# Optimization experiments

Hardware: AMD Instinct MI355X
Metric: run time of the kernel (lower is better)

Reference implementation:

```python
import jax, jax.numpy as jnp
import numpy as np

N = 32768
DEG = 9        # 8 neighbors + self-loop
B = 8
K = 3          # Chebyshev degree
IN_CH = 8
OUT_CH = 2
HID = 64


def setup_inputs() -> dict:
    key = jax.random.key(0)
    ks = jax.random.split(key, 14)
    # structured 9-neighbor stencil (CSR-like sorted rows), honoring graph sparsity
    offs = np.arange(-4, 5)
    rows_np = np.repeat(np.arange(N), DEG).astype(np.int32)
    cols_np = ((rows_np.reshape(N, DEG) + offs[None, :]) % N).reshape(-1).astype(np.int32)
    vals = jax.random.normal(ks[0], (N * DEG,), jnp.float32) * 0.1
    x = jax.random.normal(ks[1], (B, N, IN_CH), jnp.float32)

    def w(k, fin, fout):
        return jax.random.normal(k, (K * fin, fout), jnp.float32) * 0.05

    def b(k, fout):
        return jax.random.normal(k, (fout,), jnp.float32) * 0.01

    return dict(
        x=x, rows=jnp.asarray(rows_np), cols=jnp.asarray(cols_np), vals=vals,
        W1=w(ks[2], IN_CH, HID), b1=b(ks[3], HID),
        W2=w(ks[4], HID, HID), b2=b(ks[5], HID),
        W3=w(ks[6], HID, HID), b3=b(ks[7], HID),
        W4=w(ks[8], HID, HID), b4=b(ks[9], HID),
        W5=w(ks[10], HID, OUT_CH), b5=b(ks[11], OUT_CH),
    )


def _spmm(rows, cols, vals, x):
    # sparse Laplacian @ x ; x: [B, N, C] -> [B, N, C]
    g = x[:, cols, :] * vals[None, :, None]          # [B, nnz, C]
    g = jnp.swapaxes(g, 0, 1)                        # [nnz, B, C]
    y = jax.ops.segment_sum(g, rows, num_segments=N) # [N, B, C]
    return jnp.swapaxes(y, 0, 1)


def _cheb_conv(rows, cols, vals, x, W, b):
    # Chebyshev recursion: T0 = x, T1 = L x, Tk = 2 L T_{k-1} - T_{k-2}
    x0 = x
    xs = [x0]
    if K > 1:
        x1 = _spmm(rows, cols, vals, x0)
        xs.append(x1)
        for _ in range(K - 2):
            x2 = 2.0 * _spmm(rows, cols, vals, x1) - x0
            xs.append(x2)
            x0, x1 = x1, x2
    xk = jnp.concatenate(xs, axis=-1)                # [B, N, K*Fin]
    return jnp.einsum('bnf,fo->bno', xk, W) + b


def reference(x, rows, cols, vals, W1, b1, W2, b2, W3, b3, W4, b4, W5, b5):
    h = jax.nn.elu(_cheb_conv(rows, cols, vals, x, W1, b1))
    h = jax.nn.elu(_cheb_conv(rows, cols, vals, h, W2, b2))
    h = jax.nn.elu(_cheb_conv(rows, cols, vals, h, W3, b3))
    h = jax.nn.elu(_cheb_conv(rows, cols, vals, h, W4, b4))
    out = _cheb_conv(rows, cols, vals, h, W5, b5)    # no ELU on last layer
    return out
```

## Files before the change

kernel.cpp:

```cpp
#include <hip/hip_runtime.h>
#include <math.h>

#define N_PIX 32768
#define DEG 9
#define BATCH 8
#define TILE 64

typedef unsigned short u16;
typedef __attribute__((ext_vector_type(8))) short bf16x8;
typedef __attribute__((ext_vector_type(16))) float f32x16;

__device__ __forceinline__ u16 bf16_rn(float x) {
    unsigned int u = __builtin_bit_cast(unsigned int, x);
    u += 0x7fffu + ((u >> 16) & 1u);
    return (u16)(u >> 16);
}
__device__ __forceinline__ float bf16_to_f(u16 u) {
    unsigned int v = ((unsigned int)u) << 16;
    return __builtin_bit_cast(float, v);
}


__global__ void prep_wt(const float* __restrict__ W2, const float* __restrict__ W3,
                        const float* __restrict__ W4, u16* __restrict__ out) {
    const float* W = (blockIdx.x == 0) ? W2 : (blockIdx.x == 1) ? W3 : W4;
    u16* o = out + (size_t)blockIdx.x * 24576;
    const int base = blockIdx.y * 768;
    for (int idx = base + threadIdx.x; idx < base + 768; idx += 256) {
        int j = idx & 7;
        int lane = (idx >> 3) & 63;
        int rest = idx >> 9;
        int s = rest & 3, tt = rest >> 2;
        int mt = tt & 1, mat = tt >> 1;
        int k = s * 16 + (lane >> 5) * 8 + j;
        int m = mt * 32 + (lane & 31);
        float x = (mat == 0) ? W[k * 64 + m] - W[(128 + k) * 64 + m]
                : (mat == 1) ? W[(64 + k) * 64 + m]
                             : W[(128 + k) * 64 + m];
        u16 hi = bf16_rn(x);
        o[idx] = hi;
        o[12288 + idx] = bf16_rn(x - bf16_to_f(hi));
    }
}

__global__ void prep_w1(const float* __restrict__ W1, u16* __restrict__ out) {
    u16* o = out + 73728;
    const int base = blockIdx.x * 1536;
    for (int e = base + threadIdx.x; e < base + 1536 && e < 24576; e += 256) {
        int j = e & 7;
        int lane = (e >> 3) & 63;
        int tt = e >> 12;
        int mt = tt & 1, mat = tt >> 1;
        int m = mt * 32 + (lane & 31);
        float x = 0.f;
        if ((lane >> 5) == 0) {
            x = (mat == 0) ? W1[j * 64 + m] - W1[(16 + j) * 64 + m]
              : (mat == 1) ? W1[(8 + j) * 64 + m]
                           : W1[(16 + j) * 64 + m];
        }
        u16 hi = bf16_rn(x);
        o[e] = hi;
        o[24576 + e] = bf16_rn(x - bf16_to_f(hi));
    }
}

template<bool FIRST>
__global__ __launch_bounds__(512, 4)
void cheb_conv(const float* __restrict__ Xf, const u16* __restrict__ Xh,
               const u16* __restrict__ Xl, const float* __restrict__ vals,
               const u16* __restrict__ wt, int wbase, const float* __restrict__ bias,
               u16* __restrict__ Yh, u16* __restrict__ Yl) {
    __shared__ alignas(16) float P2s[80 * 68];
    __shared__ alignas(16) float P1s[72 * 68];
    __shared__ alignas(16) float P0s[64 * 68];
    __shared__ alignas(16) float Vs[72 * 12];

    const int tid = threadIdx.x;
    const int n0 = blockIdx.x * TILE;
    const int b  = blockIdx.y;
    const size_t bplane = (size_t)b * ((size_t)N_PIX * 64);

    for (int i = tid; i < 648; i += 512) {
        int sr = i / 9, j = i - sr * 9;
        int g = (n0 - 4 + sr) & (N_PIX - 1);
        Vs[sr * 12 + j] = vals[(size_t)g * DEG + j];
    }

    {
        const int w = tid >> 6, lane = tid & 63;
        const int half = lane >> 5, m31 = lane & 31;
        int mat, ntile, rowoff; float* dst;
        if (w < 3)      { mat = 2; ntile = (w == 0) ? 0 : ((w == 1) ? 32 : 48); rowoff = -8; dst = P2s; }
        else if (w < 6) { mat = 1; ntile = (w == 3) ? 0 : ((w == 4) ? 32 : 40); rowoff = -4; dst = P1s; }
        else            { mat = 0; ntile = (w == 6) ? 0 : 32;                   rowoff =  0; dst = P0s; }
        const int rl = ntile + m31;
        const int g = (n0 + rowoff + rl) & (N_PIX - 1);
        f32x16 acc0 = {}, acc1 = {};
        constexpr int SC   = FIRST ? 1 : 4;
        constexpr int LOFF = FIRST ? 24576 : 12288;
        const u16* a0p = wt + wbase + lane * 8 +
                         (FIRST ? (mat * 2) * 4096 : (mat * 2) * 4 * 512);
        const u16* a1p = a0p + (FIRST ? 4096 : 2048);
        const size_t bbase = bplane + (size_t)(g >> 5) * 2048 + (g & 31) * 8;
        const float* xfp = FIRST ? (Xf + (size_t)b * N_PIX * 8 + (size_t)g * 8) : nullptr;
        #pragma unroll
        for (int s = 0; s < SC; ++s) {
            bf16x8 bh = {}, bl = {};
            if constexpr (FIRST) {
                if (half == 0) {
                    float xv[8];
                    *(float4*)&xv[0] = *(const float4*)&xfp[0];
                    *(float4*)&xv[4] = *(const float4*)&xfp[4];
                    #pragma unroll
                    for (int e = 0; e < 8; ++e) {
                        u16 hh = bf16_rn(xv[e]);
                        bh[e] = (short)hh;
                        bl[e] = (short)bf16_rn(xv[e] - bf16_to_f(hh));
                    }
                }
            } else {
                const size_t off = bbase + (size_t)(s * 2 + half) * 256;
                bh = *(const bf16x8*)&Xh[off];
                bl = *(const bf16x8*)&Xl[off];
            }
            bf16x8 a0h = *(const bf16x8*)(a0p + s * 512);
            bf16x8 a0l = *(const bf16x8*)(a0p + s * 512 + LOFF);
            bf16x8 a1h = *(const bf16x8*)(a1p + s * 512);
            bf16x8 a1l = *(const bf16x8*)(a1p + s * 512 + LOFF);
            acc0 = __builtin_amdgcn_mfma_f32_32x32x16_bf16(a0l, bh, acc0, 0, 0, 0);
            acc0 = __builtin_amdgcn_mfma_f32_32x32x16_bf16(a0h, bl, acc0, 0, 0, 0);
            acc0 = __builtin_amdgcn_mfma_f32_32x32x16_bf16(a0h, bh, acc0, 0, 0, 0);
            acc1 = __builtin_amdgcn_mfma_f32_32x32x16_bf16(a1l, bh, acc1, 0, 0, 0);
            acc1 = __builtin_amdgcn_mfma_f32_32x32x16_bf16(a1h, bl, acc1, 0, 0, 0);
            acc1 = __builtin_amdgcn_mfma_f32_32x32x16_bf16(a1h, bh, acc1, 0, 0, 0);
        }
        #pragma unroll
        for (int q = 0; q < 4; ++q) {
            float4 v0 = {acc0[4 * q], acc0[4 * q + 1], acc0[4 * q + 2], acc0[4 * q + 3]};
            float4 v1 = {acc1[4 * q], acc1[4 * q + 1], acc1[4 * q + 2], acc1[4 * q + 3]};
            *(float4*)&dst[rl * 68 + q * 8 + half * 4]      = v0;
            *(float4*)&dst[rl * 68 + 32 + q * 8 + half * 4] = v1;
        }
    }
    __syncthreads();

    if (tid < 384) {
        const int st = tid >> 4, c0 = (tid & 15) << 2;
        const int r0 = st * 3;
        float4 win[11];
        #pragma unroll
        for (int l = 0; l < 11; ++l)
            win[l] = *(const float4*)&P2s[(r0 + l) * 68 + c0];
        #pragma unroll
        for (int r = 0; r < 3; ++r) {
            const int sg = r0 + r;
            float4 vA = *(const float4*)&Vs[sg * 12];
            float4 vB = *(const float4*)&Vs[sg * 12 + 4];
            float v8 = Vs[sg * 12 + 8];
            const float vj[9] = {vA.x, vA.y, vA.z, vA.w, vB.x, vB.y, vB.z, vB.w, v8};
            float4 a = {0.f, 0.f, 0.f, 0.f};
            #pragma unroll
            for (int j = 0; j < 9; ++j) {
                float4 xv = win[r + j];
                a.x = fmaf(vj[j], xv.x, a.x); a.y = fmaf(vj[j], xv.y, a.y);
                a.z = fmaf(vj[j], xv.z, a.z); a.w = fmaf(vj[j], xv.w, a.w);
            }
            float4 p1 = *(const float4*)&P1s[sg * 68 + c0];
            p1.x = fmaf(2.f, a.x, p1.x); p1.y = fmaf(2.f, a.y, p1.y);
            p1.z = fmaf(2.f, a.z, p1.z); p1.w = fmaf(2.f, a.w, p1.w);
            *(float4*)&P1s[sg * 68 + c0] = p1;
        }
    }
    __syncthreads();

    {
        const int st = tid >> 4, cx = tid & 15;
        const int y0 = st * 2, c0 = cx << 2;
        float4 win[10];
        #pragma unroll
        for (int l = 0; l < 10; ++l)
            win[l] = *(const float4*)&P1s[(y0 + l) * 68 + c0];
        const float4 bb = *(const float4*)&bias[c0];
        #pragma unroll
        for (int r = 0; r < 2; ++r) {
            const int y = y0 + r;
            float4 vA = *(const float4*)&Vs[(y + 4) * 12];
            float4 vB = *(const float4*)&Vs[(y + 4) * 12 + 4];
            float v8 = Vs[(y + 4) * 12 + 8];
            const float vj[9] = {vA.x, vA.y, vA.z, vA.w, vB.x, vB.y, vB.z, vB.w, v8};
            float4 a = bb;
            #pragma unroll
            for (int j = 0; j < 9; ++j) {
                float4 xv = win[r + j];
                a.x = fmaf(vj[j], xv.x, a.x); a.y = fmaf(vj[j], xv.y, a.y);
                a.z = fmaf(vj[j], xv.z, a.z); a.w = fmaf(vj[j], xv.w, a.w);
            }
            float4 p0 = *(const float4*)&P0s[y * 68 + c0];
            float yv[4] = {a.x + p0.x, a.y + p0.y, a.z + p0.z, a.w + p0.w};
            ushort4 h, l;
            u16 hh;
            #pragma unroll
            for (int e = 0; e < 4; ++e)
                yv[e] = yv[e] > 0.f ? yv[e] : expm1f(yv[e]);
            hh = bf16_rn(yv[0]); h.x = hh; l.x = bf16_rn(yv[0] - bf16_to_f(hh));
            hh = bf16_rn(yv[1]); h.y = hh; l.y = bf16_rn(yv[1] - bf16_to_f(hh));
            hh = bf16_rn(yv[2]); h.z = hh; l.z = bf16_rn(yv[2] - bf16_to_f(hh));
            hh = bf16_rn(yv[3]); h.w = hh; l.w = bf16_rn(yv[3] - bf16_to_f(hh));
            const int g = n0 + y;
            size_t dst = bplane + (size_t)(g >> 5) * 2048 + (size_t)(cx >> 1) * 256
                       + (g & 31) * 8 + (cx & 1) * 4;
            *(ushort4*)&Yh[dst] = h;
            *(ushort4*)&Yl[dst] = l;
        }
    }
}

__global__ __launch_bounds__(256, 4)
void cheb_last3(const u16* __restrict__ Xh, const u16* __restrict__ Xl,
                const float* __restrict__ vals,
                const float* __restrict__ W5, const float* __restrict__ b5,
                float* __restrict__ Y) {
    __shared__ alignas(16) float Pb[80 * 8];
    __shared__ alignas(16) float Sb[72 * 2];
    __shared__ alignas(16) float Vs[72 * 12];

    const int tid = threadIdx.x;
    const int n0 = blockIdx.x * TILE;
    const int b  = blockIdx.y;
    const size_t bplane = (size_t)b * ((size_t)N_PIX * 64);

    for (int i = tid; i < 648; i += 256) {
        int sr = i / 9, j = i - sr * 9;
        int g = (n0 - 4 + sr) & (N_PIX - 1);
        Vs[sr * 12 + j] = vals[(size_t)g * DEG + j];
    }

    {
        const int w = tid >> 6, lane = tid & 63;
        const int half = lane >> 5, m31 = lane & 31;
        if (w < 3) {
            const int ntile = (w == 0) ? 0 : ((w == 1) ? 32 : 48);
            const int rl = ntile + m31;
            const int g = (n0 - 8 + rl) & (N_PIX - 1);
            const size_t bbase = bplane + (size_t)(g >> 5) * 2048 + (g & 31) * 8;
            const bool valid = m31 < 6;
            const int seg = m31 >> 1, o = m31 & 1;
            f32x16 acc = {};
            #pragma unroll
            for (int s = 0; s < 4; ++s) {
                const size_t off = bbase + (size_t)(s * 2 + half) * 256;
                bf16x8 bh = *(const bf16x8*)&Xh[off];
                bf16x8 bl = *(const bf16x8*)&Xl[off];
                bf16x8 ah, al;
                #pragma unroll
                for (int j = 0; j < 8; ++j) {
                    int k = s * 16 + half * 8 + j;
                    float x = valid ? W5[(seg * 64 + k) * 2 + o] : 0.f;
                    u16 hh = bf16_rn(x);
                    ah[j] = (short)hh;
                    al[j] = (short)bf16_rn(x - bf16_to_f(hh));
                }
                acc = __builtin_amdgcn_mfma_f32_32x32x16_bf16(al, bh, acc, 0, 0, 0);
                acc = __builtin_amdgcn_mfma_f32_32x32x16_bf16(ah, bl, acc, 0, 0, 0);
                acc = __builtin_amdgcn_mfma_f32_32x32x16_bf16(ah, bh, acc, 0, 0, 0);
            }
            if (half == 0) {
                float4 v = {acc[0], acc[1], acc[2], acc[3]};
                *(float4*)&Pb[rl * 8] = v;
            } else {
                Pb[rl * 8 + 4] = acc[0];
                Pb[rl * 8 + 5] = acc[1];
            }
        }
    }
    __syncthreads();

    if (tid < 144) {
        const int sg = tid >> 1, o = tid & 1;
        float q = 0.f;
        #pragma unroll
        for (int j = 0; j < DEG; ++j)
            q = fmaf(Vs[sg * 12 + j], Pb[(sg + j) * 8 + 4 + o], q);
        Sb[sg * 2 + o] = Pb[(sg + 4) * 8 + 2 + o] + 2.f * q;
    }
    __syncthreads();

    if (tid < 128) {
        const int y = tid >> 1, o = tid & 1;
        float q = 0.f;
        #pragma unroll
        for (int j = 0; j < DEG; ++j)
            q = fmaf(Vs[(y + 4) * 12 + j], Sb[(y + j) * 2 + o], q);
        float v = Pb[(y + 8) * 8 + o] - Pb[(y + 8) * 8 + 4 + o] + q + b5[o];
        Y[((size_t)b * N_PIX + n0 + y) * 2 + o] = v;
    }
}

extern "C" void kernel_launch(void* const* d_in, const int* in_sizes, int n_in,
                              void* d_out, int out_size, void* d_ws, size_t ws_size,
                              hipStream_t stream) {
    const float* x    = (const float*)d_in[0];
    const float* vals = (const float*)d_in[3];
    const float* W1 = (const float*)d_in[4];
    const float* b1 = (const float*)d_in[5];
    const float* W2 = (const float*)d_in[6];
    const float* b2 = (const float*)d_in[7];
    const float* W3 = (const float*)d_in[8];
    const float* b3 = (const float*)d_in[9];
    const float* W4 = (const float*)d_in[10];
    const float* b4 = (const float*)d_in[11];
    const float* W5 = (const float*)d_in[12];
    const float* b5 = (const float*)d_in[13];
    float* out = (float*)d_out;

    const size_t PL = (size_t)BATCH * N_PIX * 64;
    u16* Ah_g = (u16*)d_ws;
    u16* Al_g = Ah_g + PL;
    u16* Bh_g = Ah_g + 2 * PL;
    u16* Bl_g = Ah_g + 3 * PL;
    u16* wt = (u16*)d_out;

    dim3 grid(N_PIX / TILE, BATCH);
    prep_wt<<<dim3(3, 16), dim3(256), 0, stream>>>(W2, W3, W4, wt);
    prep_w1<<<dim3(16), dim3(256), 0, stream>>>(W1, wt);
    cheb_conv<true><<<grid, dim3(512), 0, stream>>>(x, nullptr, nullptr, vals, wt, 73728, b1, Ah_g, Al_g);
    cheb_conv<false><<<grid, dim3(512), 0, stream>>>(nullptr, Ah_g, Al_g, vals, wt, 0,     b2, Bh_g, Bl_g);
    cheb_conv<false><<<grid, dim3(512), 0, stream>>>(nullptr, Bh_g, Bl_g, vals, wt, 24576, b3, Ah_g, Al_g);
    cheb_conv<false><<<grid, dim3(512), 0, stream>>>(nullptr, Ah_g, Al_g, vals, wt, 49152, b4, Bh_g, Bl_g);
    cheb_last3<<<grid, dim3(256), 0, stream>>>(Bh_g, Bl_g, vals, W5, b5, out);
}
```

Measured before the change: 319.3 us.

## Loop over batch inside each block with next-batch input prefetch and padded LDS

Each block now handles all 8 batch items for its pixel tile, so the grid shrinks from 4096 blocks to 512. The stencil values and per-thread setup are loaded once per tile instead of once per batch item. The next batch's input rows are loaded into registers while the current batch runs its MFMA and stencil stages. The LDS row stride goes from 68 to 76 floats to change the bank pattern. The ELU uses __expf-1 instead of expm1f, and the bf16 high part is now truncated instead of rounded. The smaller grid gives far fewer blocks per CU and more barriers per block, and the ELU change may cost some accuracy for small negative inputs.

```diff
diff --git a/kernel.cpp b/kernel.cpp
--- a/kernel.cpp
+++ b/kernel.cpp
@@ -70,15 +70,14 @@
                const u16* __restrict__ Xl, const float* __restrict__ vals,
                const u16* __restrict__ wt, int wbase, const float* __restrict__ bias,
                u16* __restrict__ Yh, u16* __restrict__ Yl) {
-    __shared__ alignas(16) float P2s[80 * 68];
-    __shared__ alignas(16) float P1s[72 * 68];
-    __shared__ alignas(16) float P0s[64 * 68];
+    constexpr int LD = 76;
+    __shared__ alignas(16) float P2s[80 * LD];
+    __shared__ alignas(16) float P1s[72 * LD];
+    __shared__ alignas(16) float P0s[64 * LD];
     __shared__ alignas(16) float Vs[72 * 12];
 
     const int tid = threadIdx.x;
     const int n0 = blockIdx.x * TILE;
-    const int b  = blockIdx.y;
-    const size_t bplane = (size_t)b * ((size_t)N_PIX * 64);
 
     for (int i = tid; i < 648; i += 512) {
         int sr = i / 9, j = i - sr * 9;
@@ -86,132 +85,161 @@
         Vs[sr * 12 + j] = vals[(size_t)g * DEG + j];
     }
 
-    {
-        const int w = tid >> 6, lane = tid & 63;
-        const int half = lane >> 5, m31 = lane & 31;
-        int mat, ntile, rowoff; float* dst;
-        if (w < 3)      { mat = 2; ntile = (w == 0) ? 0 : ((w == 1) ? 32 : 48); rowoff = -8; dst = P2s; }
-        else if (w < 6) { mat = 1; ntile = (w == 3) ? 0 : ((w == 4) ? 32 : 40); rowoff = -4; dst = P1s; }
-        else            { mat = 0; ntile = (w == 6) ? 0 : 32;                   rowoff =  0; dst = P0s; }
-        const int rl = ntile + m31;
-        const int g = (n0 + rowoff + rl) & (N_PIX - 1);
-        f32x16 acc0 = {}, acc1 = {};
-        constexpr int SC   = FIRST ? 1 : 4;
-        constexpr int LOFF = FIRST ? 24576 : 12288;
-        const u16* a0p = wt + wbase + lane * 8 +
-                         (FIRST ? (mat * 2) * 4096 : (mat * 2) * 4 * 512);
-        const u16* a1p = a0p + (FIRST ? 4096 : 2048);
-        const size_t bbase = bplane + (size_t)(g >> 5) * 2048 + (g & 31) * 8;
-        const float* xfp = FIRST ? (Xf + (size_t)b * N_PIX * 8 + (size_t)g * 8) : nullptr;
-        #pragma unroll
-        for (int s = 0; s < SC; ++s) {
-            bf16x8 bh = {}, bl = {};
-            if constexpr (FIRST) {
-                if (half == 0) {
-                    float xv[8];
-                    *(float4*)&xv[0] = *(const float4*)&xfp[0];
-                    *(float4*)&xv[4] = *(const float4*)&xfp[4];
-                    #pragma unroll
-                    for (int e = 0; e < 8; ++e) {
-                        u16 hh = bf16_rn(xv[e]);
-                        bh[e] = (short)hh;
-                        bl[e] = (short)bf16_rn(xv[e] - bf16_to_f(hh));
+    const int w = tid >> 6, lane = tid & 63;
+    const int half = lane >> 5, m31 = lane & 31;
+    int mat, ntile, rowoff; float* dst;
+    if (w < 3)      { mat = 2; ntile = (w == 0) ? 0 : ((w == 1) ? 32 : 48); rowoff = -8; dst = P2s; }
+    else if (w < 6) { mat = 1; ntile = (w == 3) ? 0 : ((w == 4) ? 32 : 40); rowoff = -4; dst = P1s; }
+    else            { mat = 0; ntile = (w == 6) ? 0 : 32;                   rowoff =  0; dst = P0s; }
+    const int rl = ntile + m31;
+    const int g = (n0 + rowoff + rl) & (N_PIX - 1);
+    const size_t rowchunk = (size_t)(g >> 5) * 2048 + (size_t)(g & 31) * 8 + (size_t)half * 256;
+    constexpr int SC   = FIRST ? 1 : 4;
+    constexpr int LOFF = FIRST ? 24576 : 12288;
+    const u16* a0p = wt + wbase + lane * 8 + (FIRST ? (mat * 2) * 4096 : mat * 4096);
+    const u16* a1p = a0p + (FIRST ? 4096 : 2048);
+
+    const int est = tid >> 4, ecx = tid & 15;
+    const int ey0 = est * 2, ec0 = ecx << 2;
+    const float4 bb = *(const float4*)&bias[ec0];
+    const size_t echunk0 = (size_t)(ecx >> 1) * 256 + (size_t)(ecx & 1) * 4;
+
+    bf16x8 nbh[SC], nbl[SC];
+    float4 nx0 = {0,0,0,0}, nx1 = {0,0,0,0};
+
+    auto prefetch = [&](int bt) {
+        if constexpr (FIRST) {
+            if (half == 0) {
+                const float* xfp = Xf + ((size_t)bt * N_PIX + g) * 8;
+                nx0 = *(const float4*)&xfp[0];
+                nx1 = *(const float4*)&xfp[4];
+            }
+        } else {
+            const u16* ph = Xh + (size_t)bt * ((size_t)N_PIX * 64) + rowchunk;
+            const u16* pl = Xl + (size_t)bt * ((size_t)N_PIX * 64) + rowchunk;
+            #pragma unroll
+            for (int s = 0; s < SC; ++s) {
+                nbh[s] = *(const bf16x8*)(ph + s * 512);
+                nbl[s] = *(const bf16x8*)(pl + s * 512);
+            }
+        }
+    };
+    prefetch(0);
+
+    for (int bt = 0; bt < BATCH; ++bt) {
+        {
+            f32x16 acc0 = {}, acc1 = {};
+            #pragma unroll
+            for (int s = 0; s < SC; ++s) {
+                bf16x8 bh, bl;
+                if constexpr (FIRST) {
+                    bh = bf16x8{}; bl = bf16x8{};
+                    if (half == 0) {
+                        float xv[8] = {nx0.x, nx0.y, nx0.z, nx0.w, nx1.x, nx1.y, nx1.z, nx1.w};
+                        #pragma unroll
+                        for (int e = 0; e < 8; ++e) {
+                            u16 hh = bf16_rn(xv[e]);
+                            bh[e] = (short)hh;
+                            bl[e] = (short)bf16_rn(xv[e] - bf16_to_f(hh));
+                        }
                     }
+                } else {
+                    bh = nbh[s]; bl = nbl[s];
                 }
-            } else {
-                const size_t off = bbase + (size_t)(s * 2 + half) * 256;
-                bh = *(const bf16x8*)&Xh[off];
-                bl = *(const bf16x8*)&Xl[off];
-            }
-            bf16x8 a0h = *(const bf16x8*)(a0p + s * 512);
-            bf16x8 a0l = *(const bf16x8*)(a0p + s * 512 + LOFF);
-            bf16x8 a1h = *(const bf16x8*)(a1p + s * 512);
-            bf16x8 a1l = *(const bf16x8*)(a1p + s * 512 + LOFF);
-            acc0 = __builtin_amdgcn_mfma_f32_32x32x16_bf16(a0l, bh, acc0, 0, 0, 0);
-            acc0 = __builtin_amdgcn_mfma_f32_32x32x16_bf16(a0h, bl, acc0, 0, 0, 0);
-            acc0 = __builtin_amdgcn_mfma_f32_32x32x16_bf16(a0h, bh, acc0, 0, 0, 0);
-            acc1 = __builtin_amdgcn_mfma_f32_32x32x16_bf16(a1l, bh, acc1, 0, 0, 0);
-            acc1 = __builtin_amdgcn_mfma_f32_32x32x16_bf16(a1h, bl, acc1, 0, 0, 0);
-            acc1 = __builtin_amdgcn_mfma_f32_32x32x16_bf16(a1h, bh, acc1, 0, 0, 0);
-        }
-        #pragma unroll
-        for (int q = 0; q < 4; ++q) {
-            float4 v0 = {acc0[4 * q], acc0[4 * q + 1], acc0[4 * q + 2], acc0[4 * q + 3]};
-            float4 v1 = {acc1[4 * q], acc1[4 * q + 1], acc1[4 * q + 2], acc1[4 * q + 3]};
-            *(float4*)&dst[rl * 68 + q * 8 + half * 4]      = v0;
-            *(float4*)&dst[rl * 68 + 32 + q * 8 + half * 4] = v1;
-        }
-    }
-    __syncthreads();
-
-    if (tid < 384) {
-        const int st = tid >> 4, c0 = (tid & 15) << 2;
-        const int r0 = st * 3;
-        float4 win[11];
-        #pragma unroll
-        for (int l = 0; l < 11; ++l)
-            win[l] = *(const float4*)&P2s[(r0 + l) * 68 + c0];
-        #pragma unroll
-        for (int r = 0; r < 3; ++r) {
-            const int sg = r0 + r;
-            float4 vA = *(const float4*)&Vs[sg * 12];
-            float4 vB = *(const float4*)&Vs[sg * 12 + 4];
-            float v8 = Vs[sg * 12 + 8];
-            const float vj[9] = {vA.x, vA.y, vA.z, vA.w, vB.x, vB.y, vB.z, vB.w, v8};
-            float4 a = {0.f, 0.f, 0.f, 0.f};
-            #pragma unroll
-            for (int j = 0; j < 9; ++j) {
-                float4 xv = win[r + j];
-                a.x = fmaf(vj[j], xv.x, a.x); a.y = fmaf(vj[j], xv.y, a.y);
-                a.z = fmaf(vj[j], xv.z, a.z); a.w = fmaf(vj[j], xv.w, a.w);
-            }
-            float4 p1 = *(const float4*)&P1s[sg * 68 + c0];
-            p1.x = fmaf(2.f, a.x, p1.x); p1.y = fmaf(2.f, a.y, p1.y);
-            p1.z = fmaf(2.f, a.z, p1.z); p1.w = fmaf(2.f, a.w, p1.w);
-            *(float4*)&P1s[sg * 68 + c0] = p1;
-        }
-    }
-    __syncthreads();
-
-    {
-        const int st = tid >> 4, cx = tid & 15;
-        const int y0 = st * 2, c0 = cx << 2;
-        float4 win[10];
-        #pragma unroll
-        for (int l = 0; l < 10; ++l)
-            win[l] = *(const float4*)&P1s[(y0 + l) * 68 + c0];
-        const float4 bb = *(const float4*)&bias[c0];
-        #pragma unroll
-        for (int r = 0; r < 2; ++r) {
-            const int y = y0 + r;
-            float4 vA = *(const float4*)&Vs[(y + 4) * 12];
-            float4 vB = *(const float4*)&Vs[(y + 4) * 12 + 4];
-            float v8 = Vs[(y + 4) * 12 + 8];
-            const float vj[9] = {vA.x, vA.y, vA.z, vA.w, vB.x, vB.y, vB.z, vB.w, v8};
-            float4 a = bb;
-            #pragma unroll
-            for (int j = 0; j < 9; ++j) {
-                float4 xv = win[r + j];
-                a.x = fmaf(vj[j], xv.x, a.x); a.y = fmaf(vj[j], xv.y, a.y);
-                a.z = fmaf(vj[j], xv.z, a.z); a.w = fmaf(vj[j], xv.w, a.w);
-            }
-            float4 p0 = *(const float4*)&P0s[y * 68 + c0];
-            float yv[4] = {a.x + p0.x, a.y + p0.y, a.z + p0.z, a.w + p0.w};
-            ushort4 h, l;
-            u16 hh;
-            #pragma unroll
-            for (int e = 0; e < 4; ++e)
-                yv[e] = yv[e] > 0.f ? yv[e] : expm1f(yv[e]);
-            hh = bf16_rn(yv[0]); h.x = hh; l.x = bf16_rn(yv[0] - bf16_to_f(hh));
-            hh = bf16_rn(yv[1]); h.y = hh; l.y = bf16_rn(yv[1] - bf16_to_f(hh));
-            hh = bf16_rn(yv[2]); h.z = hh; l.z = bf16_rn(yv[2] - bf16_to_f(hh));
-            hh = bf16_rn(yv[3]); h.w = hh; l.w = bf16_rn(yv[3] - bf16_to_f(hh));
-            const int g = n0 + y;
-            size_t dst = bplane + (size_t)(g >> 5) * 2048 + (size_t)(cx >> 1) * 256
-                       + (g & 31) * 8 + (cx & 1) * 4;
-            *(ushort4*)&Yh[dst] = h;
-            *(ushort4*)&Yl[dst] = l;
-        }
+                bf16x8 a0h = *(const bf16x8*)(a0p + s * 512);
+                bf16x8 a0l = *(const bf16x8*)(a0p + s * 512 + LOFF);
+                bf16x8 a1h = *(const bf16x8*)(a1p + s * 512);
+                bf16x8 a1l = *(const bf16x8*)(a1p + s * 512 + LOFF);
+                acc0 = __builtin_amdgcn_mfma_f32_32x32x16_bf16(a0l, bh, acc0, 0, 0, 0);
+                acc0 = __builtin_amdgcn_mfma_f32_32x32x16_bf16(a0h, bl, acc0, 0, 0, 0);
+                acc0 = __builtin_amdgcn_mfma_f32_32x32x16_bf16(a0h, bh, acc0, 0, 0, 0);
+                acc1 = __builtin_amdgcn_mfma_f32_32x32x16_bf16(a1l, bh, acc1, 0, 0, 0);
+                acc1 = __builtin_amdgcn_mfma_f32_32x32x16_bf16(a1h, bl, acc1, 0, 0, 0);
+                acc1 = __builtin_amdgcn_mfma_f32_32x32x16_bf16(a1h, bh, acc1, 0, 0, 0);
+            }
+            if (bt + 1 < BATCH) prefetch(bt + 1);
+            #pragma unroll
+            for (int q = 0; q < 4; ++q) {
+                float4 v0 = {acc0[4 * q], acc0[4 * q + 1], acc0[4 * q + 2], acc0[4 * q + 3]};
+                float4 v1 = {acc1[4 * q], acc1[4 * q + 1], acc1[4 * q + 2], acc1[4 * q + 3]};
+                *(float4*)&dst[rl * LD + q * 8 + half * 4]      = v0;
+                *(float4*)&dst[rl * LD + 32 + q * 8 + half * 4] = v1;
+            }
+        }
+        __syncthreads();
+
+        if (tid < 384) {
+            const int st = tid >> 4, c0 = (tid & 15) << 2;
+            const int r0 = st * 3;
+            float4 win[11];
+            #pragma unroll
+            for (int l = 0; l < 11; ++l)
+                win[l] = *(const float4*)&P2s[(r0 + l) * LD + c0];
+            #pragma unroll
+            for (int r = 0; r < 3; ++r) {
+                const int sg = r0 + r;
+                float4 vA = *(const float4*)&Vs[sg * 12];
+                float4 vB = *(const float4*)&Vs[sg * 12 + 4];
+                float v8 = Vs[sg * 12 + 8];
+                const float vj[9] = {vA.x, vA.y, vA.z, vA.w, vB.x, vB.y, vB.z, vB.w, v8};
+                float4 a = {0.f, 0.f, 0.f, 0.f};
+                #pragma unroll
+                for (int j = 0; j < 9; ++j) {
+                    float4 xv = win[r + j];
+                    a.x = fmaf(vj[j], xv.x, a.x); a.y = fmaf(vj[j], xv.y, a.y);
+                    a.z = fmaf(vj[j], xv.z, a.z); a.w = fmaf(vj[j], xv.w, a.w);
+                }
+                float4 p1 = *(const float4*)&P1s[sg * LD + c0];
+                p1.x = fmaf(2.f, a.x, p1.x); p1.y = fmaf(2.f, a.y, p1.y);
+                p1.z = fmaf(2.f, a.z, p1.z); p1.w = fmaf(2.f, a.w, p1.w);
+                *(float4*)&P1s[sg * LD + c0] = p1;
+            }
+        }
+        __syncthreads();
+
+        {
+            float4 win[10];
+            #pragma unroll
+            for (int l = 0; l < 10; ++l)
+                win[l] = *(const float4*)&P1s[(ey0 + l) * LD + ec0];
+            #pragma unroll
+            for (int r = 0; r < 2; ++r) {
+                const int y = ey0 + r;
+                float4 vA = *(const float4*)&Vs[(y + 4) * 12];
+                float4 vB = *(const float4*)&Vs[(y + 4) * 12 + 4];
+                float v8 = Vs[(y + 4) * 12 + 8];
+                const float vj[9] = {vA.x, vA.y, vA.z, vA.w, vB.x, vB.y, vB.z, vB.w, v8};
+                float4 a = bb;
+                #pragma unroll
+                for (int j = 0; j < 9; ++j) {
+                    float4 xv = win[r + j];
+                    a.x = fmaf(vj[j], xv.x, a.x); a.y = fmaf(vj[j], xv.y, a.y);
+                    a.z = fmaf(vj[j], xv.z, a.z); a.w = fmaf(vj[j], xv.w, a.w);
+                }
+                float4 p0 = *(const float4*)&P0s[y * LD + ec0];
+                float yv[4] = {a.x + p0.x, a.y + p0.y, a.z + p0.z, a.w + p0.w};
+                #pragma unroll
+                for (int e = 0; e < 4; ++e)
+                    yv[e] = yv[e] > 0.f ? yv[e] : __expf(yv[e]) - 1.f;
+                ushort4 h, l;
+                unsigned int u0 = __builtin_bit_cast(unsigned int, yv[0]);
+                unsigned int u1 = __builtin_bit_cast(unsigned int, yv[1]);
+                unsigned int u2 = __builtin_bit_cast(unsigned int, yv[2]);
+                unsigned int u3 = __builtin_bit_cast(unsigned int, yv[3]);
+                h.x = (u16)(u0 >> 16); h.y = (u16)(u1 >> 16);
+                h.z = (u16)(u2 >> 16); h.w = (u16)(u3 >> 16);
+                l.x = bf16_rn(yv[0] - __builtin_bit_cast(float, u0 & 0xffff0000u));
+                l.y = bf16_rn(yv[1] - __builtin_bit_cast(float, u1 & 0xffff0000u));
+                l.z = bf16_rn(yv[2] - __builtin_bit_cast(float, u2 & 0xffff0000u));
+                l.w = bf16_rn(yv[3] - __builtin_bit_cast(float, u3 & 0xffff0000u));
+                const int gy = n0 + y;
+                size_t dsto = (size_t)bt * ((size_t)N_PIX * 64)
+                            + (size_t)(gy >> 5) * 2048 + (size_t)(gy & 31) * 8 + echunk0;
+                *(ushort4*)&Yh[dsto] = h;
+                *(ushort4*)&Yl[dsto] = l;
+            }
+        }
+        __syncthreads();
     }
 }
 
@@ -320,12 +348,11 @@
     u16* Bl_g = Ah_g + 3 * PL;
     u16* wt = (u16*)d_out;
 
-    dim3 grid(N_PIX / TILE, BATCH);
     prep_wt<<<dim3(3, 16), dim3(256), 0, stream>>>(W2, W3, W4, wt);
     prep_w1<<<dim3(16), dim3(256), 0, stream>>>(W1, wt);
-    cheb_conv<true><<<grid, dim3(512), 0, stream>>>(x, nullptr, nullptr, vals, wt, 73728, b1, Ah_g, Al_g);
-    cheb_conv<false><<<grid, dim3(512), 0, stream>>>(nullptr, Ah_g, Al_g, vals, wt, 0,     b2, Bh_g, Bl_g);
-    cheb_conv<false><<<grid, dim3(512), 0, stream>>>(nullptr, Bh_g, Bl_g, vals, wt, 24576, b3, Ah_g, Al_g);
-    cheb_conv<false><<<grid, dim3(512), 0, stream>>>(nullptr, Ah_g, Al_g, vals, wt, 49152, b4, Bh_g, Bl_g);
-    cheb_last3<<<grid, dim3(256), 0, stream>>>(Bh_g, Bl_g, vals, W5, b5, out);
-}
+    cheb_conv<true><<<dim3(512), dim3(512), 0, stream>>>(x, nullptr, nullptr, vals, wt, 73728, b1, Ah_g, Al_g);
+    cheb_conv<false><<<dim3(512), dim3(512), 0, stream>>>(nullptr, Ah_g, Al_g, vals, wt, 0,     b2, Bh_g, Bl_g);
+    cheb_conv<false><<<dim3(512), dim3(512), 0, stream>>>(nullptr, Bh_g, Bl_g, vals, wt, 24576, b3, Ah_g, Al_g);
+    cheb_conv<false><<<dim3(512), dim3(512), 0, stream>>>(nullptr, Ah_g, Al_g, vals, wt, 49152, b4, Bh_g, Bl_g);
+    cheb_last3<<<dim3(512, 8), dim3(256), 0, stream>>>(Bh_g, Bl_g, vals, W5, b5, out);
+}
```

Result: slower. 471.3 us (+47.6%).
